# Kernel optimization log

Measured on AMD Instinct MI355X. Metric: run time of the kernel, lower is better.

## Reference

```python
import jax, jax.numpy as jnp
import numpy as np

HEADS = 8

def setup_inputs() -> dict:
    key = jax.random.key(0)
    ks = jax.random.split(key, 5)
    B, S, C = 2, 4096, 640
    s = 1.0 / np.sqrt(C)
    return {
        "hidden_states": jax.random.normal(ks[0], (B, S, C), dtype=jnp.float32),
        "Wq": jax.random.normal(ks[1], (C, C), dtype=jnp.float32) * s,
        "bq": jnp.zeros((C,), dtype=jnp.float32),
        "Wk": jax.random.normal(ks[2], (C, C), dtype=jnp.float32) * s,
        "bk": jnp.zeros((C,), dtype=jnp.float32),
        "Wv": jax.random.normal(ks[3], (C, C), dtype=jnp.float32) * s,
        "bv": jnp.zeros((C,), dtype=jnp.float32),
        "Wo": jax.random.normal(ks[4], (C, C), dtype=jnp.float32) * s,
        "bo": jnp.zeros((C,), dtype=jnp.float32),
    }


def reference(hidden_states, Wq, bq, Wk, bk, Wv, bv, Wo, bo):
    # Self-attention (encoder_hidden_states=None), no mask, no norms.
    B, S, C = hidden_states.shape
    H = HEADS
    D = C // H  # head_dim
    residual = hidden_states

    q = hidden_states @ Wq + bq  # [B,S,C]
    k = hidden_states @ Wk + bk
    v = hidden_states @ Wv + bv

    # [B,S,C] -> [B,H,S,D]
    q = q.reshape(B, S, H, D).transpose(0, 2, 1, 3)
    k = k.reshape(B, S, H, D).transpose(0, 2, 1, 3)
    v = v.reshape(B, S, H, D).transpose(0, 2, 1, 3)

    scale = 1.0 / np.sqrt(D)
    scores = jnp.einsum('bhqd,bhkd->bhqk', q, k) * scale  # [B,H,S,S]
    probs = jax.nn.softmax(scores, axis=-1)               # materialized, as in source
    out = jnp.einsum('bhqk,bhkd->bhqd', probs, v)         # [B,H,S,D]

    out = out.transpose(0, 2, 1, 3).reshape(B, S, C)
    out = out @ Wo + bo  # to_out[0]; to_out[1] is dropout (identity in eval)
    out = out + residual  # residual_connection=True
    return out            # rescale_output_factor = 1.0
```

## Files before the change

kernel.cpp:

```cpp
#include <hip/hip_runtime.h>
#include <hip/hip_bf16.h>
#include <stdint.h>

typedef __attribute__((ext_vector_type(8))) short short8;
typedef __attribute__((ext_vector_type(4))) short short4v;
typedef __attribute__((ext_vector_type(4))) float f32x4;
typedef __attribute__((ext_vector_type(16))) float f32x16;
typedef unsigned short u16;
typedef unsigned int u32;

#define DEV __device__ __forceinline__

constexpr int Bb = 2, Ss = 4096, Cc = 640, Hh = 8, Dd = 80;
constexpr int BS = Bb * Ss;
constexpr int NQKV = 3 * Cc;
constexpr int QKst = 2 * Cc;

DEV float bf2f(u16 u) { unsigned v = ((unsigned)u) << 16; float f; __builtin_memcpy(&f, &v, 4); return f; }
DEV u16 f2bf(float f) {
    unsigned u; __builtin_memcpy(&u, &f, 4);
    u += 0x7fffu + ((u >> 16) & 1u);
    return (u16)(u >> 16);
}
DEV u32 packbf2(float a, float b) {
    float2 f2; f2.x = a; f2.y = b;
    __hip_bfloat162 h2 = __float22bfloat162_rn(f2);
    u32 r; __builtin_memcpy(&r, &h2, 4);
    return r;
}

DEV void pswapf(float &a, float &b) {
#if __has_builtin(__builtin_amdgcn_permlane32_swap)
    auto r = __builtin_amdgcn_permlane32_swap(__float_as_int(a), __float_as_int(b), false, false);
    a = __int_as_float(r[0]); b = __int_as_float(r[1]);
#else
    float sa = __shfl_xor(a, 32, 64), sb = __shfl_xor(b, 32, 64);
    bool hi = (threadIdx.x & 32) != 0;
    float na = hi ? sb : a, nb = hi ? b : sa;
    a = na; b = nb;
#endif
}

#define GLD16(gp, lp) __builtin_amdgcn_global_load_lds( \
    (const __attribute__((address_space(1))) void*)(gp), \
    (__attribute__((address_space(3))) void*)(lp), 16, 0, 0)

__global__ __launch_bounds__(256) void prep_kernel(
    const float* __restrict__ hs,
    const float* __restrict__ Wq, const float* __restrict__ Wk,
    const float* __restrict__ Wv, const float* __restrict__ Wo,
    const float* __restrict__ bq, const float* __restrict__ bk,
    const float* __restrict__ bv,
    u16* __restrict__ Xb, float* __restrict__ bcat,
    u16* __restrict__ WTqkv, u16* __restrict__ WTo)
{
    const float QS = 0.11180339887498949f * 1.4426950408889634f;
    if (blockIdx.x < 1600) {
        __shared__ float T[32][33];
        int tile = blockIdx.x;
        int wsel = tile / 400;
        int tt = tile - wsel * 400;
        int tr = tt / 20, tc = tt - (tt / 20) * 20;
        const float* W = (wsel == 0) ? Wq : (wsel == 1) ? Wk : (wsel == 2) ? Wv : Wo;
        float sc = (wsel == 0) ? QS : 1.0f;
        int r = threadIdx.x >> 3, c4 = (threadIdx.x & 7) * 4;
        float4 v = *(const float4*)(W + (size_t)(tr * 32 + r) * Cc + tc * 32 + c4);
        T[r][c4 + 0] = v.x; T[r][c4 + 1] = v.y; T[r][c4 + 2] = v.z; T[r][c4 + 3] = v.w;
        __syncthreads();
        short4v o;
#pragma unroll
        for (int j = 0; j < 4; j++) o[j] = (short)f2bf(T[c4 + j][r] * sc);
        u16* dst = (wsel < 3) ? (WTqkv + (size_t)(wsel * Cc + tc * 32 + r) * Cc + tr * 32 + c4)
                              : (WTo + (size_t)(tc * 32 + r) * Cc + tr * 32 + c4);
        *(short4v*)dst = o;
    } else {
        int tid = (blockIdx.x - 1600) * blockDim.x + threadIdx.x;
        int nthr = 2048 * blockDim.x;
        for (int i = tid; i < BS * Cc / 4; i += nthr) {
            float4 v = ((const float4*)hs)[i];
            short4v o;
            o[0] = (short)f2bf(v.x); o[1] = (short)f2bf(v.y);
            o[2] = (short)f2bf(v.z); o[3] = (short)f2bf(v.w);
            ((short4v*)Xb)[i] = o;
        }
        for (int i = tid; i < NQKV; i += nthr) {
            float v = (i < Cc) ? bq[i] * QS : (i < 2 * Cc) ? bk[i - Cc] : bv[i - 2 * Cc];
            bcat[i] = v;
        }
    }
}

__global__ __launch_bounds__(256) void gemm_qkv(
    const u16* __restrict__ A, const u16* __restrict__ Bt,
    const float* __restrict__ bias, u16* __restrict__ QK,
    u16* __restrict__ VTg)
{
    constexpr int BKP = 40;
    __shared__ __align__(16) u16 As[128 * BKP];
    __shared__ __align__(16) u16 Bs[128 * BKP];

    const int mBase = blockIdx.x * 128;
    const int nBase = blockIdx.y * 128;
    const int t = threadIdx.x, lane = t & 63, w = t >> 6;
    const int wr = w >> 1, wc = w & 1;
    const int l15 = lane & 15, g = lane >> 4;

    f32x4 acc[4][4] = {};
    const int rowA = t >> 1;
    const int colA = (t & 1) * 16;

    for (int k0 = 0; k0 < Cc; k0 += 32) {
        const u16* pa = A + (size_t)(mBase + rowA) * Cc + k0 + colA;
        const u16* pb = Bt + (size_t)(nBase + rowA) * Cc + k0 + colA;
        short8 a0 = *(const short8*)pa;
        short8 a1 = *(const short8*)(pa + 8);
        short8 b0 = *(const short8*)pb;
        short8 b1 = *(const short8*)(pb + 8);
        *(short8*)&As[rowA * BKP + colA] = a0;
        *(short8*)&As[rowA * BKP + colA + 8] = a1;
        *(short8*)&Bs[rowA * BKP + colA] = b0;
        *(short8*)&Bs[rowA * BKP + colA + 8] = b1;
        __syncthreads();
        short8 af[4], bf[4];
#pragma unroll
        for (int i = 0; i < 4; i++) {
            af[i] = *(const short8*)&As[(wr * 64 + i * 16 + l15) * BKP + g * 8];
            bf[i] = *(const short8*)&Bs[(wc * 64 + i * 16 + l15) * BKP + g * 8];
        }
#pragma unroll
        for (int mi = 0; mi < 4; mi++)
#pragma unroll
            for (int ni = 0; ni < 4; ni++)
                acc[mi][ni] = __builtin_amdgcn_mfma_f32_16x16x32_bf16(af[mi], bf[ni], acc[mi][ni], 0, 0, 0);
        __syncthreads();
    }

    if (nBase < 2 * Cc) {
#pragma unroll
        for (int mi = 0; mi < 4; mi++)
#pragma unroll
            for (int ni = 0; ni < 4; ni++) {
                int col = nBase + wc * 64 + ni * 16 + l15;
                float bb = bias[col];
#pragma unroll
                for (int r = 0; r < 4; r++) {
                    int row = mBase + wr * 64 + mi * 16 + g * 4 + r;
                    QK[(size_t)row * QKst + col] = f2bf(acc[mi][ni][r] + bb);
                }
            }
    } else {
        const int gp = ((g & 1) << 1) | (g >> 1);
#pragma unroll
        for (int mi = 0; mi < 4; mi++)
#pragma unroll
            for (int ni = 0; ni < 4; ni++) {
                int colg = nBase + wc * 64 + ni * 16 + l15;
                float bb = bias[colg];
                int vc = colg - 2 * Cc;
                int h = vc / Dd, d = vc - h * Dd;
                int row0 = mBase + wr * 64 + mi * 16 + gp * 4;
                int b = (mBase >> 12), s = row0 & 4095;
                short4v o;
#pragma unroll
                for (int r = 0; r < 4; r++) o[r] = (short)f2bf(acc[mi][ni][r] + bb);
                *(short4v*)(VTg + ((size_t)(b * Hh + h) * Dd + d) * Ss + s) = o;
            }
    }
}

constexpr int OBP = 88;

__global__ __launch_bounds__(256, 4) void attn_kernel(
    const u16* __restrict__ QK, const u16* __restrict__ VTg,
    u16* __restrict__ N0, u16* __restrict__ N1,
    float* __restrict__ Mp, float* __restrict__ Lp)
{
    __shared__ __align__(16) char smem[34816];

    const int id = blockIdx.x;
    const int qt = id >> 5;
    const int bh = (id & 31) >> 1;
    const int kvs = id & 1;
    const int b = bh >> 3, h = bh & 7;
    const int t = threadIdx.x, lane = t & 63, w = t >> 6;
    const int l31 = lane & 31, e = lane >> 5;

    const size_t rowBase = (size_t)b * Ss;
    const int q0 = qt * 128;
    const int kvBase = kvs * (Ss / 2);
    constexpr int NT = (Ss / 2) / 64;

    const int lq8 = lane >> 3;
    const int vcg = (lane & 7) ^ lq8;
    const u16* kg0 = QK + (rowBase + kvBase + lane) * QKst + Cc + h * Dd;
    const u16* vg0 = VTg + ((size_t)bh * Dd) * Ss + kvBase + vcg * 8;

    for (int i = t; i < 512; i += 256) {
        ((u32*)(smem + 10240 + 80 * 128))[i] = 0x3F803F80u;
        ((u32*)(smem + 10240 + 12288 + 80 * 128))[i] = 0x3F803F80u;
    }

    short8 qB[5];
    {
        const u16* qp = QK + (rowBase + q0 + w * 32 + l31) * QKst + h * Dd + e * 8;
#pragma unroll
        for (int ks = 0; ks < 5; ks++) qB[ks] = *(const short8*)(qp + ks * 16);
    }

    auto stageK = [&](int kt) {
#pragma unroll
        for (int j = 0; j < 3; j++) {
            int gi = w + 4 * j;
            if (gi < 10)
                GLD16(kg0 + (size_t)kt * 64 * QKst + gi * 8, smem + gi * 1024);
        }
    };
    auto stageV = [&](int kt, int vb) {
#pragma unroll
        for (int j = 0; j < 3; j++) {
            int gi = w + 4 * j;
            if (gi < 10)
                GLD16(vg0 + (size_t)(gi * 8 + lq8) * Ss + kt * 64,
                      smem + 10240 + vb * 12288 + gi * 1024);
        }
    };

    stageK(0);
    stageV(0, 0);
    __syncthreads();

    float mrow = -1e30f;
    f32x16 oacc[3] = {};
    int vcur = 0;
    const int csl_base = l31 & 7;

    for (int kt = 0; kt < NT; ++kt) {
        const bool more = (kt + 1 < NT);

        f32x16 s2[2];
        __builtin_amdgcn_s_setprio(1);
#pragma unroll
        for (int n = 0; n < 2; n++) {
            f32x16 a = {};
#pragma unroll
            for (int ks = 0; ks < 5; ks++) {
                short8 kf = *(const short8*)(smem + ((2 * ks + e) * 64 + n * 32 + l31) * 16);
                a = __builtin_amdgcn_mfma_f32_32x32x16_bf16(kf, qB[ks], a, 0, 0, 0);
            }
            s2[n] = a;
        }
        __builtin_amdgcn_s_setprio(0);

        __syncthreads();
        if (more) {
            stageK(kt + 1);
            stageV(kt + 1, vcur ^ 1);
        }

#define SV(j) ((j) < 16 ? s2[0][(j)] : s2[1][(j) - 16])
        float tt[11];
#pragma unroll
        for (int i = 0; i < 10; i++)
            tt[i] = fmaxf(fmaxf(SV(3 * i), SV(3 * i + 1)), SV(3 * i + 2));
        tt[10] = fmaxf(SV(30), SV(31));
#undef SV
        float u0 = fmaxf(fmaxf(tt[0], tt[1]), tt[2]);
        float u1 = fmaxf(fmaxf(tt[3], tt[4]), tt[5]);
        float u2 = fmaxf(fmaxf(tt[6], tt[7]), tt[8]);
        float u3 = fmaxf(tt[9], tt[10]);
        float vm = fmaxf(fmaxf(u0, u1), fmaxf(u2, u3));
        { float va = vm, vb = vm; pswapf(va, vb); vm = fmaxf(va, vb); }

        if (__any(vm > mrow + 8.0f)) {
            float mnew = fmaxf(mrow, vm);
            float al = __builtin_amdgcn_exp2f(mrow - mnew);
            mrow = mnew;
#pragma unroll
            for (int n = 0; n < 3; n++)
#pragma unroll
                for (int r = 0; r < 16; r++) oacc[n][r] *= al;
        }

        u32 pd[2][8];
#pragma unroll
        for (int n = 0; n < 2; n++)
#pragma unroll
            for (int m = 0; m < 8; m++) {
                float pa = __builtin_amdgcn_exp2f(s2[n][2 * m] - mrow);
                float pb = __builtin_amdgcn_exp2f(s2[n][2 * m + 1] - mrow);
                pd[n][m] = packbf2(pa, pb);
            }

        const char* vbase = smem + 10240 + vcur * 12288;
        __builtin_amdgcn_s_setprio(1);
#pragma unroll
        for (int ks = 0; ks < 4; ks++) {
            const int n = ks >> 1, bb2 = ks & 1;
            union { u32 u[4]; short8 v; } pB;
            pB.u[0] = pd[n][4 * bb2 + 0];
            pB.u[1] = pd[n][4 * bb2 + 1];
            pB.u[2] = pd[n][4 * bb2 + 2];
            pB.u[3] = pd[n][4 * bb2 + 3];
            const int csl = (2 * ks + e) ^ csl_base;
#pragma unroll
            for (int n2 = 0; n2 < 3; n2++) {
                short8 vf = *(const short8*)(vbase + ((n2 * 32 + l31) * 8 + csl) * 16);
                oacc[n2] = __builtin_amdgcn_mfma_f32_32x32x16_bf16(vf, pB.v, oacc[n2], 0, 0, 0);
            }
        }
        __builtin_amdgcn_s_setprio(0);

        __syncthreads();
        vcur ^= 1;
    }

    if (e == 0) {
        int mi = kvs * 65536 + bh * Ss + q0 + w * 32 + l31;
        Mp[mi] = mrow;
        Lp[mi] = oacc[2][8];
    }

    u16* Ob = (u16*)smem;
#pragma unroll
    for (int n = 0; n < 3; n++)
#pragma unroll
        for (int r = 0; r < 16; r += 2) {
            if (n == 2 && r >= 8) continue;
            int dloc = n * 32 + (r & 3) + 8 * (r >> 2) + 4 * e;
            u32 pk = packbf2(oacc[n][r], oacc[n][r + 1]);
            *(u32*)&Ob[(w * 32 + l31) * OBP + dloc] = pk;
        }
    __syncthreads();

    u16* Np = kvs ? N1 : N0;
    const int cb = h * Dd;
#pragma unroll
    for (int i = 0; i < 5; i++) {
        int gidx = i * 256 + t;
        int row = gidx / 10, gi = gidx % 10;
        short8 v = *(const short8*)&Ob[row * OBP + gi * 8];
        *(short8*)(Np + (rowBase + q0 + row) * Cc + cb + gi * 8) = v;
    }
}

__global__ __launch_bounds__(256) void gemm_oproj(
    const u16* __restrict__ N0, const u16* __restrict__ N1,
    const u16* __restrict__ Bt,
    const float* __restrict__ Mp, const float* __restrict__ Lp,
    const float* __restrict__ bias, const float* __restrict__ resid,
    float* __restrict__ Out)
{
    constexpr int BKP = 40;
    __shared__ __align__(16) u16 As[128 * BKP];
    __shared__ __align__(16) u16 Bs[128 * BKP];
    __shared__ float WF[128][8][2];

    const int mBase = blockIdx.x * 128;
    const int nBase = blockIdx.y * 128;
    const int t = threadIdx.x, lane = t & 63, w = t >> 6;
    const int wr = w >> 1, wc = w & 1;
    const int l15 = lane & 15, g = lane >> 4;

    for (int i = t; i < 1024; i += 256) {
        int r = i >> 3, h = i & 7;
        int row = mBase + r;
        int bb = row >> 12, q = row & 4095;
        int mi = (bb * 8 + h) * Ss + q;
        float m0 = Mp[mi], m1 = Mp[65536 + mi];
        float l0 = Lp[mi], l1 = Lp[65536 + mi];
        float m = fmaxf(m0, m1);
        float w0 = exp2f(m0 - m), w1 = exp2f(m1 - m);
        float rl = 1.0f / (l0 * w0 + l1 * w1);
        WF[r][h][0] = w0 * rl;
        WF[r][h][1] = w1 * rl;
    }
    __syncthreads();

    f32x4 acc[4][4] = {};
    const int rowA = t >> 1;
    const int colA = (t & 1) * 16;

    for (int k0 = 0; k0 < Cc; k0 += 32) {
        const int kc = k0 + colA;
        const int hh = kc / 80;
        float w0 = WF[rowA][hh][0], w1 = WF[rowA][hh][1];
        const u16* p0 = N0 + (size_t)(mBase + rowA) * Cc + kc;
        const u16* p1 = N1 + (size_t)(mBase + rowA) * Cc + kc;
        short8 a0 = *(const short8*)p0;
        short8 a1 = *(const short8*)(p0 + 8);
        short8 c0 = *(const short8*)p1;
        short8 c1 = *(const short8*)(p1 + 8);
        u32 mg[8];
#pragma unroll
        for (int j = 0; j < 4; j++) {
            mg[j] = packbf2(bf2f((u16)a0[2 * j]) * w0 + bf2f((u16)c0[2 * j]) * w1,
                            bf2f((u16)a0[2 * j + 1]) * w0 + bf2f((u16)c0[2 * j + 1]) * w1);
            mg[4 + j] = packbf2(bf2f((u16)a1[2 * j]) * w0 + bf2f((u16)c1[2 * j]) * w1,
                                bf2f((u16)a1[2 * j + 1]) * w0 + bf2f((u16)c1[2 * j + 1]) * w1);
        }
        const u16* pb = Bt + (size_t)(nBase + rowA) * Cc + kc;
        short8 b0 = *(const short8*)pb;
        short8 b1 = *(const short8*)(pb + 8);
#pragma unroll
        for (int j = 0; j < 4; j++) {
            *(u32*)&As[rowA * BKP + colA + 2 * j] = mg[j];
            *(u32*)&As[rowA * BKP + colA + 8 + 2 * j] = mg[4 + j];
        }
        *(short8*)&Bs[rowA * BKP + colA] = b0;
        *(short8*)&Bs[rowA * BKP + colA + 8] = b1;
        __syncthreads();
        short8 af[4], bf[4];
#pragma unroll
        for (int i = 0; i < 4; i++) {
            af[i] = *(const short8*)&As[(wr * 64 + i * 16 + l15) * BKP + g * 8];
            bf[i] = *(const short8*)&Bs[(wc * 64 + i * 16 + l15) * BKP + g * 8];
        }
#pragma unroll
        for (int mi = 0; mi < 4; mi++)
#pragma unroll
            for (int ni = 0; ni < 4; ni++)
                acc[mi][ni] = __builtin_amdgcn_mfma_f32_16x16x32_bf16(af[mi], bf[ni], acc[mi][ni], 0, 0, 0);
        __syncthreads();
    }

#pragma unroll
    for (int mi = 0; mi < 4; mi++)
#pragma unroll
        for (int ni = 0; ni < 4; ni++) {
            int col = nBase + wc * 64 + ni * 16 + l15;
            float bb = bias[col];
#pragma unroll
            for (int r = 0; r < 4; r++) {
                int row = mBase + wr * 64 + mi * 16 + g * 4 + r;
                Out[(size_t)row * Cc + col] = acc[mi][ni][r] + bb + resid[(size_t)row * Cc + col];
            }
        }
}

extern "C" void kernel_launch(void* const* d_in, const int* in_sizes, int n_in,
                              void* d_out, int out_size, void* d_ws, size_t ws_size,
                              hipStream_t stream) {
    (void)in_sizes; (void)n_in; (void)out_size; (void)ws_size;
    const float* hs = (const float*)d_in[0];
    const float* Wq = (const float*)d_in[1];
    const float* bq = (const float*)d_in[2];
    const float* Wk = (const float*)d_in[3];
    const float* bk = (const float*)d_in[4];
    const float* Wv = (const float*)d_in[5];
    const float* bv = (const float*)d_in[6];
    const float* Wo = (const float*)d_in[7];
    const float* bo = (const float*)d_in[8];
    float* out = (float*)d_out;

    char* ws = (char*)d_ws;
    u16*   Xb    = (u16*)  (ws + 0);
    u16*   WTqkv = (u16*)  (ws + 10485760);
    u16*   WTo   = (u16*)  (ws + 12943360);
    float* bcat  = (float*)(ws + 13762560);
    u16*   QK    = (u16*)  (ws + 13770240);
    u16*   VTg   = (u16*)  (ws + 34741760);
    u16*   AOb   = (u16*)  (ws + 45227520);
    float* Mp    = (float*)(ws + 55713280);
    float* Lp    = (float*)(ws + 56237568);
    u16*   N1    = Xb;

    prep_kernel<<<dim3(3648), dim3(256), 0, stream>>>(hs, Wq, Wk, Wv, Wo, bq, bk, bv,
                                                      Xb, bcat, WTqkv, WTo);
    gemm_qkv<<<dim3(64, 15), dim3(256), 0, stream>>>(Xb, WTqkv, bcat, QK, VTg);
    attn_kernel<<<dim3(1024), dim3(256), 0, stream>>>(QK, VTg, AOb, N1, Mp, Lp);
    gemm_oproj<<<dim3(64, 5), dim3(256), 0, stream>>>(AOb, N1, WTo, Mp, Lp, bo, hs, out);
}
```

Baseline: 200.7 us.

## Double-buffer QKV and output GEMMs with direct global-to-LDS loads and swizzle

Both projection GEMMs now stage tiles through double-buffered shared memory. Tiles are loaded with a GLD16 helper (presumably global-to-LDS direct loads) into an XOR-swizzled layout with no padding, so the next k-slice loads while MFMAs run on the current one. The output projection also halves its M tile to 64 rows, doubling the grid to give the GPU more blocks. Its split-merge of the two attention partials is interleaved after the MFMAs. This is meant to hide global load latency and remove one barrier per k-step, at the cost of more complex indexing and reliance on GLD16, which is defined outside the shown code.

```diff
diff --git a/kernel.cpp b/kernel.cpp
--- a/kernel.cpp
+++ b/kernel.cpp
@@ -95,9 +95,7 @@
     const float* __restrict__ bias, u16* __restrict__ QK,
     u16* __restrict__ VTg)
 {
-    constexpr int BKP = 40;
-    __shared__ __align__(16) u16 As[128 * BKP];
-    __shared__ __align__(16) u16 Bs[128 * BKP];
+    __shared__ __align__(16) char gsm[32768];
 
     const int mBase = blockIdx.x * 128;
     const int nBase = blockIdx.y * 128;
@@ -105,27 +103,35 @@
     const int wr = w >> 1, wc = w & 1;
     const int l15 = lane & 15, g = lane >> 4;
 
+    const int r0 = t >> 2, r1 = (t + 256) >> 2;
+    const int cg0 = (t & 3) ^ (r0 & 3);
+    const int cg1 = (t & 3) ^ (r1 & 3);
+    const u16* pa0 = A + (size_t)(mBase + r0) * Cc + cg0 * 8;
+    const u16* pa1 = A + (size_t)(mBase + r1) * Cc + cg1 * 8;
+    const u16* pb0 = Bt + (size_t)(nBase + r0) * Cc + cg0 * 8;
+    const u16* pb1 = Bt + (size_t)(nBase + r1) * Cc + cg1 * 8;
+
+    auto stage = [&](int k0, int buf) {
+        GLD16(pa0 + k0, gsm + buf * 8192 + w * 1024);
+        GLD16(pa1 + k0, gsm + buf * 8192 + 4096 + w * 1024);
+        GLD16(pb0 + k0, gsm + 16384 + buf * 8192 + w * 1024);
+        GLD16(pb1 + k0, gsm + 16384 + buf * 8192 + 4096 + w * 1024);
+    };
+
+    stage(0, 0);
+    __syncthreads();
+
     f32x4 acc[4][4] = {};
-    const int rowA = t >> 1;
-    const int colA = (t & 1) * 16;
+    const int lof = l15 * 64 + ((g ^ (l15 & 3)) << 4);
+    int cur = 0;
 
     for (int k0 = 0; k0 < Cc; k0 += 32) {
-        const u16* pa = A + (size_t)(mBase + rowA) * Cc + k0 + colA;
-        const u16* pb = Bt + (size_t)(nBase + rowA) * Cc + k0 + colA;
-        short8 a0 = *(const short8*)pa;
-        short8 a1 = *(const short8*)(pa + 8);
-        short8 b0 = *(const short8*)pb;
-        short8 b1 = *(const short8*)(pb + 8);
-        *(short8*)&As[rowA * BKP + colA] = a0;
-        *(short8*)&As[rowA * BKP + colA + 8] = a1;
-        *(short8*)&Bs[rowA * BKP + colA] = b0;
-        *(short8*)&Bs[rowA * BKP + colA + 8] = b1;
-        __syncthreads();
+        if (k0 + 32 < Cc) stage(k0 + 32, cur ^ 1);
         short8 af[4], bf[4];
 #pragma unroll
         for (int i = 0; i < 4; i++) {
-            af[i] = *(const short8*)&As[(wr * 64 + i * 16 + l15) * BKP + g * 8];
-            bf[i] = *(const short8*)&Bs[(wc * 64 + i * 16 + l15) * BKP + g * 8];
+            af[i] = *(const short8*)(gsm + cur * 8192 + wr * 4096 + i * 1024 + lof);
+            bf[i] = *(const short8*)(gsm + 16384 + cur * 8192 + wc * 4096 + i * 1024 + lof);
         }
 #pragma unroll
         for (int mi = 0; mi < 4; mi++)
@@ -133,6 +139,7 @@
             for (int ni = 0; ni < 4; ni++)
                 acc[mi][ni] = __builtin_amdgcn_mfma_f32_16x16x32_bf16(af[mi], bf[ni], acc[mi][ni], 0, 0, 0);
         __syncthreads();
+        cur ^= 1;
     }
 
     if (nBase < 2 * Cc) {
@@ -350,18 +357,16 @@
     const float* __restrict__ bias, const float* __restrict__ resid,
     float* __restrict__ Out)
 {
-    constexpr int BKP = 40;
-    __shared__ __align__(16) u16 As[128 * BKP];
-    __shared__ __align__(16) u16 Bs[128 * BKP];
-    __shared__ float WF[128][8][2];
-
-    const int mBase = blockIdx.x * 128;
+    __shared__ __align__(16) char osm[28672];
+    float* WF = (float*)(osm + 24576);
+
+    const int mBase = blockIdx.x * 64;
     const int nBase = blockIdx.y * 128;
     const int t = threadIdx.x, lane = t & 63, w = t >> 6;
     const int wr = w >> 1, wc = w & 1;
     const int l15 = lane & 15, g = lane >> 4;
 
-    for (int i = t; i < 1024; i += 256) {
+    for (int i = t; i < 512; i += 256) {
         int r = i >> 3, h = i & 7;
         int row = mBase + r;
         int bb = row >> 12, q = row & 4095;
@@ -371,67 +376,76 @@
         float m = fmaxf(m0, m1);
         float w0 = exp2f(m0 - m), w1 = exp2f(m1 - m);
         float rl = 1.0f / (l0 * w0 + l1 * w1);
-        WF[r][h][0] = w0 * rl;
-        WF[r][h][1] = w1 * rl;
-    }
+        WF[(r * 8 + h) * 2 + 0] = w0 * rl;
+        WF[(r * 8 + h) * 2 + 1] = w1 * rl;
+    }
+
+    const int rA = t >> 2, clA = t & 3;
+    const int cgA = clA ^ (rA & 3);
+    const int rB0 = t >> 2, rB1 = (t + 256) >> 2;
+    const int cgB0 = (t & 3) ^ (rB0 & 3);
+    const int cgB1 = (t & 3) ^ (rB1 & 3);
+    const u16* pA0 = N0 + (size_t)(mBase + rA) * Cc + cgA * 8;
+    const u16* pA1 = N1 + (size_t)(mBase + rA) * Cc + cgA * 8;
+    const u16* pB0 = Bt + (size_t)(nBase + rB0) * Cc + cgB0 * 8;
+    const u16* pB1 = Bt + (size_t)(nBase + rB1) * Cc + cgB1 * 8;
+
+    auto stageB = [&](int k0, int buf) {
+        GLD16(pB0 + k0, osm + 8192 + buf * 8192 + w * 1024);
+        GLD16(pB1 + k0, osm + 8192 + buf * 8192 + 4096 + w * 1024);
+    };
+    auto stageA = [&](int k0, int buf) {
+        int kA = k0 + cgA * 8;
+        int hA = kA / 80;
+        float w0 = WF[(rA * 8 + hA) * 2], w1 = WF[(rA * 8 + hA) * 2 + 1];
+        short8 a0 = *(const short8*)(pA0 + k0);
+        short8 c0 = *(const short8*)(pA1 + k0);
+        union { u32 u[4]; short8 v; } mg;
+#pragma unroll
+        for (int j = 0; j < 4; j++)
+            mg.u[j] = packbf2(bf2f((u16)a0[2 * j]) * w0 + bf2f((u16)c0[2 * j]) * w1,
+                              bf2f((u16)a0[2 * j + 1]) * w0 + bf2f((u16)c0[2 * j + 1]) * w1);
+        *(short8*)(osm + buf * 4096 + rA * 64 + clA * 16) = mg.v;
+    };
+
     __syncthreads();
-
-    f32x4 acc[4][4] = {};
-    const int rowA = t >> 1;
-    const int colA = (t & 1) * 16;
+    stageB(0, 0);
+    stageA(0, 0);
+    __syncthreads();
+
+    f32x4 acc[2][4] = {};
+    const int lof = l15 * 64 + ((g ^ (l15 & 3)) << 4);
+    int cur = 0;
 
     for (int k0 = 0; k0 < Cc; k0 += 32) {
-        const int kc = k0 + colA;
-        const int hh = kc / 80;
-        float w0 = WF[rowA][hh][0], w1 = WF[rowA][hh][1];
-        const u16* p0 = N0 + (size_t)(mBase + rowA) * Cc + kc;
-        const u16* p1 = N1 + (size_t)(mBase + rowA) * Cc + kc;
-        short8 a0 = *(const short8*)p0;
-        short8 a1 = *(const short8*)(p0 + 8);
-        short8 c0 = *(const short8*)p1;
-        short8 c1 = *(const short8*)(p1 + 8);
-        u32 mg[8];
-#pragma unroll
-        for (int j = 0; j < 4; j++) {
-            mg[j] = packbf2(bf2f((u16)a0[2 * j]) * w0 + bf2f((u16)c0[2 * j]) * w1,
-                            bf2f((u16)a0[2 * j + 1]) * w0 + bf2f((u16)c0[2 * j + 1]) * w1);
-            mg[4 + j] = packbf2(bf2f((u16)a1[2 * j]) * w0 + bf2f((u16)c1[2 * j]) * w1,
-                                bf2f((u16)a1[2 * j + 1]) * w0 + bf2f((u16)c1[2 * j + 1]) * w1);
-        }
-        const u16* pb = Bt + (size_t)(nBase + rowA) * Cc + kc;
-        short8 b0 = *(const short8*)pb;
-        short8 b1 = *(const short8*)(pb + 8);
-#pragma unroll
-        for (int j = 0; j < 4; j++) {
-            *(u32*)&As[rowA * BKP + colA + 2 * j] = mg[j];
-            *(u32*)&As[rowA * BKP + colA + 8 + 2 * j] = mg[4 + j];
-        }
-        *(short8*)&Bs[rowA * BKP + colA] = b0;
-        *(short8*)&Bs[rowA * BKP + colA + 8] = b1;
-        __syncthreads();
-        short8 af[4], bf[4];
-#pragma unroll
-        for (int i = 0; i < 4; i++) {
-            af[i] = *(const short8*)&As[(wr * 64 + i * 16 + l15) * BKP + g * 8];
-            bf[i] = *(const short8*)&Bs[(wc * 64 + i * 16 + l15) * BKP + g * 8];
-        }
-#pragma unroll
-        for (int mi = 0; mi < 4; mi++)
+        const bool more = (k0 + 32 < Cc);
+        if (more) stageB(k0 + 32, cur ^ 1);
+        short8 af[2], bf[4];
+#pragma unroll
+        for (int i = 0; i < 2; i++)
+            af[i] = *(const short8*)(osm + cur * 4096 + wr * 2048 + i * 1024 + lof);
+#pragma unroll
+        for (int i = 0; i < 4; i++)
+            bf[i] = *(const short8*)(osm + 8192 + cur * 8192 + wc * 4096 + i * 1024 + lof);
+#pragma unroll
+        for (int mi = 0; mi < 2; mi++)
 #pragma unroll
             for (int ni = 0; ni < 4; ni++)
                 acc[mi][ni] = __builtin_amdgcn_mfma_f32_16x16x32_bf16(af[mi], bf[ni], acc[mi][ni], 0, 0, 0);
+        if (more) stageA(k0 + 32, cur ^ 1);
         __syncthreads();
-    }
-
-#pragma unroll
-    for (int mi = 0; mi < 4; mi++)
+        cur ^= 1;
+    }
+
+#pragma unroll
+    for (int mi = 0; mi < 2; mi++)
 #pragma unroll
         for (int ni = 0; ni < 4; ni++) {
             int col = nBase + wc * 64 + ni * 16 + l15;
             float bb = bias[col];
 #pragma unroll
             for (int r = 0; r < 4; r++) {
-                int row = mBase + wr * 64 + mi * 16 + g * 4 + r;
+                int row = mBase + wr * 32 + mi * 16 + g * 4 + r;
                 Out[(size_t)row * Cc + col] = acc[mi][ni][r] + bb + resid[(size_t)row * Cc + col];
             }
         }
@@ -468,5 +482,5 @@
                                                       Xb, bcat, WTqkv, WTo);
     gemm_qkv<<<dim3(64, 15), dim3(256), 0, stream>>>(Xb, WTqkv, bcat, QK, VTg);
     attn_kernel<<<dim3(1024), dim3(256), 0, stream>>>(QK, VTg, AOb, N1, Mp, Lp);
-    gemm_oproj<<<dim3(64, 5), dim3(256), 0, stream>>>(AOb, N1, WTo, Mp, Lp, bo, hs, out);
-}
+    gemm_oproj<<<dim3(128, 5), dim3(256), 0, stream>>>(AOb, N1, WTo, Mp, Lp, bo, hs, out);
+}
```

After: 184.3 us, median of 2. 1.09x faster.
